# Kernel optimization log

Hardware: AMD Instinct MI355X
Metric: run time of the kernel (lower is better)

Reference implementation:

```python
import jax, jax.numpy as jnp
import numpy as np

NUM_USER = 100000
NUM_ITEM = 50000
EMBED_DIM = 64
NUM_LAYER = 3
NUM_INTERACTIONS = 1600000  # symmetrized -> nnz = 3.2M
BATCH = 4096


def setup_inputs() -> dict:
    key = jax.random.key(0)
    k1, k2, k3, k4, k5, k6 = jax.random.split(key, 6)
    N = NUM_USER + NUM_ITEM
    user_emb = jax.random.normal(k1, (NUM_USER, EMBED_DIM), dtype=jnp.float32) / EMBED_DIM
    item_emb = jax.random.normal(k2, (NUM_ITEM, EMBED_DIM), dtype=jnp.float32) / EMBED_DIM
    # random bipartite interactions, symmetrized adjacency
    u = jax.random.randint(k3, (NUM_INTERACTIONS,), 0, NUM_USER, dtype=jnp.int32)
    i = jax.random.randint(k4, (NUM_INTERACTIONS,), 0, NUM_ITEM, dtype=jnp.int32) + NUM_USER
    adj_rows = jnp.concatenate([u, i])  # [nnz]
    adj_cols = jnp.concatenate([i, u])  # [nnz]
    # symmetric normalization D^-1/2 A D^-1/2
    deg = jax.ops.segment_sum(jnp.ones_like(adj_rows, dtype=jnp.float32), adj_rows, num_segments=N)
    deg = jnp.maximum(deg, 1.0)
    inv_sqrt = 1.0 / jnp.sqrt(deg)
    adj_vals = inv_sqrt[adj_rows] * inv_sqrt[adj_cols]
    user_ids = jax.random.randint(k5, (BATCH,), 0, NUM_USER, dtype=jnp.int32)
    item_ids = jax.random.randint(k6, (BATCH,), 0, NUM_ITEM, dtype=jnp.int32)
    return {"user_emb": user_emb, "item_emb": item_emb, "adj_vals": adj_vals,
            "adj_rows": adj_rows, "adj_cols": adj_cols,
            "user_ids": user_ids, "item_ids": item_ids}


def reference(user_emb, item_emb, adj_vals, adj_rows, adj_cols, user_ids, item_ids):
    num_user = user_emb.shape[0]
    N = num_user + item_emb.shape[0]
    x = jnp.concatenate([user_emb, item_emb], axis=0)  # [N, D]
    acc = x  # running sum == stack+mean over layers, fused
    for _ in range(NUM_LAYER):
        # SpMM: out[r] += vals * x[c]
        x = jax.ops.segment_sum(adj_vals[:, None] * x[adj_cols], adj_rows, num_segments=N)
        acc = acc + x
    emb = acc / (NUM_LAYER + 1)
    batch_user = emb[user_ids]                  # [B, D]
    batch_item = emb[num_user + item_ids]       # [B, D]
    scores = jnp.sum(batch_user * batch_item, axis=-1)  # DotProdScorer
    return scores
```

## Files before the change

kernel.cpp:

```cpp
#include <hip/hip_runtime.h>


#define DIM 64
#define TSHIFT 8
#define TMASK ((1 << TSHIFT) - 1)
#define TPAD 768
#define EWG 6272
#define STAGE_CAP 6272
#define TSTRIDE 10240

typedef unsigned short u16;
typedef unsigned char u8;
typedef unsigned int u32;

__device__ __forceinline__ u32 f2bf(float f) {
  u32 u = __float_as_uint(f);
  return (u + 0x7FFFu + ((u >> 16) & 1u)) >> 16;
}
__device__ __forceinline__ float bflo(u32 u) {
  return __uint_as_float(u << 16);
}
__device__ __forceinline__ float bfhi(u32 u) {
  return __uint_as_float(u & 0xFFFF0000u);
}


__global__ __launch_bounds__(256) void partition_direct(
    const int* __restrict__ rows, const int* __restrict__ cols, int nnz,
    int T, int* __restrict__ tcur, u32* __restrict__ bucket) {
  __shared__ u32 sorted[STAGE_CAP];
  __shared__ u16 sortedt[STAGE_CAP];
  __shared__ int cnt[TPAD], lstart[TPAD], cur[TPAD], gbase[TPAD];
  __shared__ int hsum[256];
  int w = blockIdx.x, tid = threadIdx.x;
  int j0 = tid * 3;
  cnt[j0] = 0; cnt[j0 + 1] = 0; cnt[j0 + 2] = 0;
  cur[j0] = 0; cur[j0 + 1] = 0; cur[j0 + 2] = 0;
  __syncthreads();
  int base = w * EWG;
  int end = min(base + EWG, nnz);
  int total = end - base;
  if (total <= 0) return;
  for (int e = base + tid; e < end; e += 256)
    atomicAdd(&cnt[rows[e] >> TSHIFT], 1);
  __syncthreads();
  int c0 = cnt[j0], c1 = cnt[j0 + 1], c2 = cnt[j0 + 2];
  int lsum = c0 + c1 + c2;
  hsum[tid] = lsum;
  __syncthreads();
  for (int off = 1; off < 256; off <<= 1) {
    int v = (tid >= off) ? hsum[tid - off] : 0;
    __syncthreads();
    hsum[tid] += v;
    __syncthreads();
  }
  int excl = hsum[tid] - lsum;
  lstart[j0] = excl;
  lstart[j0 + 1] = excl + c0;
  lstart[j0 + 2] = excl + c0 + c1;
  if (c0 > 0) gbase[j0] = j0 * TSTRIDE + atomicAdd(&tcur[j0], c0);
  if (c1 > 0) gbase[j0 + 1] = (j0 + 1) * TSTRIDE + atomicAdd(&tcur[j0 + 1], c1);
  if (c2 > 0) gbase[j0 + 2] = (j0 + 2) * TSTRIDE + atomicAdd(&tcur[j0 + 2], c2);
  __syncthreads();
  for (int e = base + tid; e < end; e += 256) {
    int r = rows[e];
    int c = cols[e];
    int t = r >> TSHIFT;
    int slot = atomicAdd(&cur[t], 1);
    int d = lstart[t] + slot;
    sorted[d] = ((u32)(r & TMASK) << 18) | (u32)c;
    sortedt[d] = (u16)t;
  }
  __syncthreads();
  for (int i = tid; i < total; i += 256) {
    int t = sortedt[i];
    bucket[(size_t)gbase[t] + (i - lstart[t])] = sorted[i];
  }
}


__global__ __launch_bounds__(256) void build_csr_y0(
    const u32* __restrict__ bucket, const int* __restrict__ tcur, int T,
    int U, int N, const float4* __restrict__ ue, const float4* __restrict__ ie,
    int* __restrict__ row_ptr, u32* __restrict__ csr,
    uint4* __restrict__ y0b) {
  __shared__ int tl[TPAD];
  __shared__ int hist[256];
  __shared__ int sc[256];
  __shared__ int cur[256];
  int b = blockIdx.x;
  int t = (b & 1) ? (T - 1 - (b >> 1)) : (b >> 1);
  int tid = threadIdx.x;
  int j0 = tid * 3;
  int v0 = (j0 < T) ? tcur[j0] : 0;
  int v1 = (j0 + 1 < T) ? tcur[j0 + 1] : 0;
  int v2 = (j0 + 2 < T) ? tcur[j0 + 2] : 0;
  int lsum = v0 + v1 + v2;
  sc[tid] = lsum;
  __syncthreads();
  for (int off = 1; off < 256; off <<= 1) {
    int v = (tid >= off) ? sc[tid - off] : 0;
    __syncthreads();
    sc[tid] += v;
    __syncthreads();
  }
  int excl = sc[tid] - lsum;
  tl[j0] = excl + v0;
  tl[j0 + 1] = excl + v0 + v1;
  tl[j0 + 2] = excl + v0 + v1 + v2;
  hist[tid] = 0;
  __syncthreads();
  int tbase = (t == 0) ? 0 : tl[t - 1];
  int tlen = tl[t] - tbase;
  int bstart = t * TSTRIDE;
  const uint4* b4 = (const uint4*)(bucket + bstart);
  int nv = tlen >> 2;
  for (int i = tid; i < nv; i += 256) {
    uint4 e = b4[i];
    atomicAdd(&hist[e.x >> 18], 1);
    atomicAdd(&hist[e.y >> 18], 1);
    atomicAdd(&hist[e.z >> 18], 1);
    atomicAdd(&hist[e.w >> 18], 1);
  }
  for (int i = bstart + (nv << 2) + tid; i < bstart + tlen; i += 256)
    atomicAdd(&hist[bucket[i] >> 18], 1);
  __syncthreads();
  int h = hist[tid];
  sc[tid] = h;
  __syncthreads();
  for (int off = 1; off < 256; off <<= 1) {
    int v = (tid >= off) ? sc[tid - off] : 0;
    __syncthreads();
    sc[tid] += v;
    __syncthreads();
  }
  int incl = sc[tid];
  int r = (t << TSHIFT) + tid;
  if (r < N) row_ptr[r + 1] = tbase + incl;
  if (t == 0 && tid == 0) row_ptr[0] = 0;
  cur[tid] = tbase + incl - h;
  __syncthreads();
  for (int pass = 0; pass < 8; ++pass) {
    int lr = pass * 32 + (tid >> 3);
    int q = tid & 7;
    int row = (t << TSHIFT) + lr;
    if (row < N) {
      float invs = rsqrtf((float)max(hist[lr], 1));
      const float4* src = (row < U) ? (ue + (size_t)row * 16 + q * 2)
                                    : (ie + (size_t)(row - U) * 16 + q * 2);
      float4 a = src[0], bb = src[1];
      uint4 o;
      o.x = f2bf(a.x * invs) | (f2bf(a.y * invs) << 16);
      o.y = f2bf(a.z * invs) | (f2bf(a.w * invs) << 16);
      o.z = f2bf(bb.x * invs) | (f2bf(bb.y * invs) << 16);
      o.w = f2bf(bb.z * invs) | (f2bf(bb.w * invs) << 16);
      y0b[(size_t)row * 8 + q] = o;
    }
  }
  for (int i = tid; i < nv; i += 256) {
    uint4 e = b4[i];
    csr[atomicAdd(&cur[e.x >> 18], 1)] = e.x & 0x3FFFFu;
    csr[atomicAdd(&cur[e.y >> 18], 1)] = e.y & 0x3FFFFu;
    csr[atomicAdd(&cur[e.z >> 18], 1)] = e.z & 0x3FFFFu;
    csr[atomicAdd(&cur[e.w >> 18], 1)] = e.w & 0x3FFFFu;
  }
  for (int i = bstart + (nv << 2) + tid; i < bstart + tlen; i += 256) {
    u32 e = bucket[i];
    csr[atomicAdd(&cur[e >> 18], 1)] = e & 0x3FFFFu;
  }
}


#define ACC8(G)                                                              \
  s0 += bflo(G.x); s1 += bfhi(G.x);                                          \
  s2 += bflo(G.y); s3 += bfhi(G.y);                                          \
  s4 += bflo(G.z); s5 += bfhi(G.z);                                          \
  s6 += bflo(G.w); s7 += bfhi(G.w);

__global__ __launch_bounds__(256) void spmm_sum(
    const int* __restrict__ row_ptr, const u32* __restrict__ csr,
    const u16* __restrict__ yin, u16* __restrict__ yout, int n) {
  if (blockIdx.x == 0 && threadIdx.x < 8)
    ((uint4*)(yout + (size_t)n * DIM))[threadIdx.x] = make_uint4(0, 0, 0, 0);
  int row = (blockIdx.x * 256 + threadIdx.x) >> 3;
  int q8 = threadIdx.x & 7;
  if (row >= n) return;
  int start = row_ptr[row];
  int end = row_ptr[row + 1];
  float s0 = 0.f, s1 = 0.f, s2 = 0.f, s3 = 0.f;
  float s4 = 0.f, s5 = 0.f, s6 = 0.f, s7 = 0.f;
  int k = start;
  for (; k + 8 <= end; k += 8) {
    u32 c0 = csr[k],     c1 = csr[k + 1], c2 = csr[k + 2], c3 = csr[k + 3];
    u32 c4 = csr[k + 4], c5 = csr[k + 5], c6 = csr[k + 6], c7 = csr[k + 7];
    uint4 g0 = ((const uint4*)(yin + (size_t)c0 * DIM))[q8];
    uint4 g1 = ((const uint4*)(yin + (size_t)c1 * DIM))[q8];
    uint4 g2 = ((const uint4*)(yin + (size_t)c2 * DIM))[q8];
    uint4 g3 = ((const uint4*)(yin + (size_t)c3 * DIM))[q8];
    uint4 g4 = ((const uint4*)(yin + (size_t)c4 * DIM))[q8];
    uint4 g5 = ((const uint4*)(yin + (size_t)c5 * DIM))[q8];
    uint4 g6 = ((const uint4*)(yin + (size_t)c6 * DIM))[q8];
    uint4 g7 = ((const uint4*)(yin + (size_t)c7 * DIM))[q8];
    ACC8(g0) ACC8(g1) ACC8(g2) ACC8(g3) ACC8(g4) ACC8(g5) ACC8(g6) ACC8(g7)
  }
  for (; k + 4 <= end; k += 4) {
    u32 c0 = csr[k], c1 = csr[k + 1], c2 = csr[k + 2], c3 = csr[k + 3];
    uint4 g0 = ((const uint4*)(yin + (size_t)c0 * DIM))[q8];
    uint4 g1 = ((const uint4*)(yin + (size_t)c1 * DIM))[q8];
    uint4 g2 = ((const uint4*)(yin + (size_t)c2 * DIM))[q8];
    uint4 g3 = ((const uint4*)(yin + (size_t)c3 * DIM))[q8];
    ACC8(g0) ACC8(g1) ACC8(g2) ACC8(g3)
  }
  for (; k < end; ++k) {
    u32 c0 = csr[k];
    uint4 g0 = ((const uint4*)(yin + (size_t)c0 * DIM))[q8];
    ACC8(g0)
  }
  float inv = 1.0f / (float)max(end - start, 1);
  uint4 o;
  o.x = f2bf(s0 * inv) | (f2bf(s1 * inv) << 16);
  o.y = f2bf(s2 * inv) | (f2bf(s3 * inv) << 16);
  o.z = f2bf(s4 * inv) | (f2bf(s5 * inv) << 16);
  o.w = f2bf(s6 * inv) | (f2bf(s7 * inv) << 16);
  ((uint4*)(yout + (size_t)row * DIM))[q8] = o;
}


__device__ __forceinline__ void gather8(
    const int* __restrict__ row_ptr, const u32* __restrict__ csr,
    const u16* __restrict__ y, int row, int s, int q8, int n, float* o) {
  int start = row_ptr[row];
  int end = row_ptr[row + 1];
  float s0 = 0.f, s1 = 0.f, s2 = 0.f, s3 = 0.f;
  float s4 = 0.f, s5 = 0.f, s6 = 0.f, s7 = 0.f;
  for (int k = start + s; k < end; k += 16) {
    int k2 = k + 8;
    bool ok2 = k2 < end;
    u32 c0 = csr[k];
    u32 c1 = ok2 ? csr[k2] : (u32)n;
    uint4 g0 = ((const uint4*)(y + (size_t)c0 * DIM))[q8];
    uint4 g1 = ((const uint4*)(y + (size_t)c1 * DIM))[q8];
    ACC8(g0) ACC8(g1)
  }
  for (int m = 8; m <= 32; m <<= 1) {
    s0 += __shfl_xor(s0, m, 64); s1 += __shfl_xor(s1, m, 64);
    s2 += __shfl_xor(s2, m, 64); s3 += __shfl_xor(s3, m, 64);
    s4 += __shfl_xor(s4, m, 64); s5 += __shfl_xor(s5, m, 64);
    s6 += __shfl_xor(s6, m, 64); s7 += __shfl_xor(s7, m, 64);
  }
  o[0] = s0; o[1] = s1; o[2] = s2; o[3] = s3;
  o[4] = s4; o[5] = s5; o[6] = s6; o[7] = s7;
}

__global__ __launch_bounds__(256) void spmm3_score(
    const int* __restrict__ row_ptr, const u32* __restrict__ csr,
    const float* __restrict__ ue, const float* __restrict__ ie,
    const u16* __restrict__ y1b, const u16* __restrict__ y2b,
    const int* __restrict__ user_ids, const int* __restrict__ item_ids,
    int U, int N, int batch, float* __restrict__ out) {
  int w = (blockIdx.x * 256 + threadIdx.x) >> 6;
  int lane = threadIdx.x & 63;
  if (w >= batch) return;
  int s = lane >> 3;
  int q8 = lane & 7;
  int u = user_ids[w];
  int iti = item_ids[w];
  int it = iti + U;
  float gu[8], gi[8];
  gather8(row_ptr, csr, y2b, u, s, q8, N, gu);
  gather8(row_ptr, csr, y2b, it, s, q8, N, gi);
  int du = row_ptr[u + 1] - row_ptr[u];
  int di = row_ptr[it + 1] - row_ptr[it];
  float su = sqrtf((float)max(du, 1)), ru = 1.0f / su;
  float si = sqrtf((float)max(di, 1)), ri = 1.0f / si;
  const float4* pu = (const float4*)(ue + (size_t)u * DIM) + q8 * 2;
  const float4* pi = (const float4*)(ie + (size_t)iti * DIM) + q8 * 2;
  float4 a0a = pu[0], a0b = pu[1];
  float4 b0a = pi[0], b0b = pi[1];
  uint4 y1u = ((const uint4*)(y1b + (size_t)u * DIM))[q8];
  uint4 y2u = ((const uint4*)(y2b + (size_t)u * DIM))[q8];
  uint4 y1i = ((const uint4*)(y1b + (size_t)it * DIM))[q8];
  uint4 y2i = ((const uint4*)(y2b + (size_t)it * DIM))[q8];
  float a[8], b[8];
  a[0] = a0a.x + su * (bflo(y1u.x) + bflo(y2u.x)) + ru * gu[0];
  a[1] = a0a.y + su * (bfhi(y1u.x) + bfhi(y2u.x)) + ru * gu[1];
  a[2] = a0a.z + su * (bflo(y1u.y) + bflo(y2u.y)) + ru * gu[2];
  a[3] = a0a.w + su * (bfhi(y1u.y) + bfhi(y2u.y)) + ru * gu[3];
  a[4] = a0b.x + su * (bflo(y1u.z) + bflo(y2u.z)) + ru * gu[4];
  a[5] = a0b.y + su * (bfhi(y1u.z) + bfhi(y2u.z)) + ru * gu[5];
  a[6] = a0b.z + su * (bflo(y1u.w) + bflo(y2u.w)) + ru * gu[6];
  a[7] = a0b.w + su * (bfhi(y1u.w) + bfhi(y2u.w)) + ru * gu[7];
  b[0] = b0a.x + si * (bflo(y1i.x) + bflo(y2i.x)) + ri * gi[0];
  b[1] = b0a.y + si * (bfhi(y1i.x) + bfhi(y2i.x)) + ri * gi[1];
  b[2] = b0a.z + si * (bflo(y1i.y) + bflo(y2i.y)) + ri * gi[2];
  b[3] = b0a.w + si * (bfhi(y1i.y) + bfhi(y2i.y)) + ri * gi[3];
  b[4] = b0b.x + si * (bflo(y1i.z) + bflo(y2i.z)) + ri * gi[4];
  b[5] = b0b.y + si * (bfhi(y1i.z) + bfhi(y2i.z)) + ri * gi[5];
  b[6] = b0b.z + si * (bflo(y1i.w) + bflo(y2i.w)) + ri * gi[6];
  b[7] = b0b.w + si * (bfhi(y1i.w) + bfhi(y2i.w)) + ri * gi[7];
  float p = 0.f;
  for (int j = 0; j < 8; ++j) p += a[j] * b[j];
  p += __shfl_xor(p, 1, 64);
  p += __shfl_xor(p, 2, 64);
  p += __shfl_xor(p, 4, 64);
  if (lane == 0) out[w] = p * (1.0f / 16.0f);
}

extern "C" void kernel_launch(void* const* d_in, const int* in_sizes, int n_in,
                              void* d_out, int out_size, void* d_ws, size_t ws_size,
                              hipStream_t stream) {
  const float* user_emb = (const float*)d_in[0];
  const float* item_emb = (const float*)d_in[1];
  const int* adj_rows = (const int*)d_in[3];
  const int* adj_cols = (const int*)d_in[4];
  const int* user_ids = (const int*)d_in[5];
  const int* item_ids = (const int*)d_in[6];
  float* scores = (float*)d_out;

  const int U = in_sizes[0] / DIM;
  const int I = in_sizes[1] / DIM;
  const int N = U + I;
  const int nnz = in_sizes[2];
  const int B = in_sizes[5];

  const int T = (N + TMASK) >> TSHIFT;
  const int npw = (nnz + EWG - 1) / EWG;

  char* p = (char*)d_ws;
  auto carve = [&](size_t bytes) {
    void* r = (void*)p;
    p += (bytes + 255) & ~(size_t)255;
    return r;
  };
  u16* y0b = (u16*)carve((size_t)(N + 1) * DIM * 2);
  u16* y1b = (u16*)carve((size_t)(N + 1) * DIM * 2);
  u16* y2b = (u16*)carve((size_t)(N + 1) * DIM * 2);
  int* row_ptr = (int*)carve((size_t)(N + 1) * 4);
  int* tcur = (int*)carve((size_t)T * 4);
  u32* bucket = (u32*)carve((size_t)(T + 1) * TSTRIDE * 4);
  u32* csr = (u32*)carve((size_t)nnz * 4);

  hipMemsetAsync(tcur, 0, (size_t)T * 4, stream);

  partition_direct<<<npw, 256, 0, stream>>>(adj_rows, adj_cols, nnz, T, tcur,
                                            bucket);

  build_csr_y0<<<T, 256, 0, stream>>>(bucket, tcur, T, U, N,
                                      (const float4*)user_emb,
                                      (const float4*)item_emb, row_ptr,
                                      csr, (uint4*)y0b);

  const int sblocks = (N * 8 + 255) / 256;
  spmm_sum<<<sblocks, 256, 0, stream>>>(row_ptr, csr, y0b, y1b, N);
  spmm_sum<<<sblocks, 256, 0, stream>>>(row_ptr, csr, y1b, y2b, N);

  spmm3_score<<<(B + 3) / 4, 256, 0, stream>>>(row_ptr, csr, user_emb,
                                               item_emb, y1b, y2b, user_ids,
                                               item_ids, U, N, B, scores);
}
```

Before: 281.7 us.

## Use wave-shuffle block scans, vectorized partition loads, and smaller partition tiles

Replaces the shared-memory Hillis-Steele block scans, which carry many barriers, with a wave-level shuffle scan plus a small cross-wave combine in both preprocessing kernels. The partition kernel now reads rows and cols as int4, reuses the count array as the slot cursor, and shrinks the per-block edge chunk from 6272 to 2560 so more blocks fit per CU (launch bounds of 5). Smaller chunks mean more blocks and more global atomics on the tile cursors, and the int4 loads assume the chunk bases stay 16-byte aligned.

```diff
diff --git a/kernel.cpp b/kernel.cpp
--- a/kernel.cpp
+++ b/kernel.cpp
@@ -5,8 +5,8 @@
 #define TSHIFT 8
 #define TMASK ((1 << TSHIFT) - 1)
 #define TPAD 768
-#define EWG 6272
-#define STAGE_CAP 6272
+#define EWG 2560
+#define STAGE_CAP 2560
 #define TSTRIDE 10240
 
 typedef unsigned short u16;
@@ -24,50 +24,84 @@
   return __uint_as_float(u & 0xFFFF0000u);
 }
 
-
-__global__ __launch_bounds__(256) void partition_direct(
+__device__ __forceinline__ int block_incl_scan(int lsum, int tid, int* wsum) {
+  int lane = tid & 63, wv = tid >> 6;
+  int v = lsum;
+#pragma unroll
+  for (int off = 1; off < 64; off <<= 1) {
+    int t = __shfl_up(v, off, 64);
+    if (lane >= off) v += t;
+  }
+  __syncthreads();
+  if (lane == 63) wsum[wv] = v;
+  __syncthreads();
+  int add = 0;
+  if (wv > 0) add += wsum[0];
+  if (wv > 1) add += wsum[1];
+  if (wv > 2) add += wsum[2];
+  return v + add;
+}
+
+
+__global__ __launch_bounds__(256, 5) void partition_direct(
     const int* __restrict__ rows, const int* __restrict__ cols, int nnz,
     int T, int* __restrict__ tcur, u32* __restrict__ bucket) {
   __shared__ u32 sorted[STAGE_CAP];
   __shared__ u16 sortedt[STAGE_CAP];
-  __shared__ int cnt[TPAD], lstart[TPAD], cur[TPAD], gbase[TPAD];
-  __shared__ int hsum[256];
+  __shared__ int cnt[TPAD], lstart[TPAD], gbase[TPAD];
+  __shared__ int wsum[4];
   int w = blockIdx.x, tid = threadIdx.x;
   int j0 = tid * 3;
   cnt[j0] = 0; cnt[j0 + 1] = 0; cnt[j0 + 2] = 0;
-  cur[j0] = 0; cur[j0 + 1] = 0; cur[j0 + 2] = 0;
   __syncthreads();
   int base = w * EWG;
   int end = min(base + EWG, nnz);
   int total = end - base;
   if (total <= 0) return;
-  for (int e = base + tid; e < end; e += 256)
+  int nv = total >> 2;
+  const int4* r4 = (const int4*)(rows + base);
+  const int4* c4 = (const int4*)(cols + base);
+  for (int i = tid; i < nv; i += 256) {
+    int4 r = r4[i];
+    atomicAdd(&cnt[r.x >> TSHIFT], 1);
+    atomicAdd(&cnt[r.y >> TSHIFT], 1);
+    atomicAdd(&cnt[r.z >> TSHIFT], 1);
+    atomicAdd(&cnt[r.w >> TSHIFT], 1);
+  }
+  for (int e = base + (nv << 2) + tid; e < end; e += 256)
     atomicAdd(&cnt[rows[e] >> TSHIFT], 1);
   __syncthreads();
   int c0 = cnt[j0], c1 = cnt[j0 + 1], c2 = cnt[j0 + 2];
   int lsum = c0 + c1 + c2;
-  hsum[tid] = lsum;
-  __syncthreads();
-  for (int off = 1; off < 256; off <<= 1) {
-    int v = (tid >= off) ? hsum[tid - off] : 0;
-    __syncthreads();
-    hsum[tid] += v;
-    __syncthreads();
-  }
-  int excl = hsum[tid] - lsum;
+  int incl = block_incl_scan(lsum, tid, wsum);
+  int excl = incl - lsum;
   lstart[j0] = excl;
   lstart[j0 + 1] = excl + c0;
   lstart[j0 + 2] = excl + c0 + c1;
   if (c0 > 0) gbase[j0] = j0 * TSTRIDE + atomicAdd(&tcur[j0], c0);
   if (c1 > 0) gbase[j0 + 1] = (j0 + 1) * TSTRIDE + atomicAdd(&tcur[j0 + 1], c1);
   if (c2 > 0) gbase[j0 + 2] = (j0 + 2) * TSTRIDE + atomicAdd(&tcur[j0 + 2], c2);
-  __syncthreads();
-  for (int e = base + tid; e < end; e += 256) {
+  cnt[j0] = 0; cnt[j0 + 1] = 0; cnt[j0 + 2] = 0;
+  __syncthreads();
+  for (int i = tid; i < nv; i += 256) {
+    int4 r = r4[i];
+    int4 c = c4[i];
+    int t, s, d;
+    t = r.x >> TSHIFT; s = atomicAdd(&cnt[t], 1); d = lstart[t] + s;
+    sorted[d] = ((u32)(r.x & TMASK) << 18) | (u32)c.x; sortedt[d] = (u16)t;
+    t = r.y >> TSHIFT; s = atomicAdd(&cnt[t], 1); d = lstart[t] + s;
+    sorted[d] = ((u32)(r.y & TMASK) << 18) | (u32)c.y; sortedt[d] = (u16)t;
+    t = r.z >> TSHIFT; s = atomicAdd(&cnt[t], 1); d = lstart[t] + s;
+    sorted[d] = ((u32)(r.z & TMASK) << 18) | (u32)c.z; sortedt[d] = (u16)t;
+    t = r.w >> TSHIFT; s = atomicAdd(&cnt[t], 1); d = lstart[t] + s;
+    sorted[d] = ((u32)(r.w & TMASK) << 18) | (u32)c.w; sortedt[d] = (u16)t;
+  }
+  for (int e = base + (nv << 2) + tid; e < end; e += 256) {
     int r = rows[e];
     int c = cols[e];
     int t = r >> TSHIFT;
-    int slot = atomicAdd(&cur[t], 1);
-    int d = lstart[t] + slot;
+    int s = atomicAdd(&cnt[t], 1);
+    int d = lstart[t] + s;
     sorted[d] = ((u32)(r & TMASK) << 18) | (u32)c;
     sortedt[d] = (u16)t;
   }
@@ -86,8 +120,8 @@
     uint4* __restrict__ y0b) {
   __shared__ int tl[TPAD];
   __shared__ int hist[256];
-  __shared__ int sc[256];
   __shared__ int cur[256];
+  __shared__ int wsum[4];
   int b = blockIdx.x;
   int t = (b & 1) ? (T - 1 - (b >> 1)) : (b >> 1);
   int tid = threadIdx.x;
@@ -96,18 +130,11 @@
   int v1 = (j0 + 1 < T) ? tcur[j0 + 1] : 0;
   int v2 = (j0 + 2 < T) ? tcur[j0 + 2] : 0;
   int lsum = v0 + v1 + v2;
-  sc[tid] = lsum;
-  __syncthreads();
-  for (int off = 1; off < 256; off <<= 1) {
-    int v = (tid >= off) ? sc[tid - off] : 0;
-    __syncthreads();
-    sc[tid] += v;
-    __syncthreads();
-  }
-  int excl = sc[tid] - lsum;
-  tl[j0] = excl + v0;
-  tl[j0 + 1] = excl + v0 + v1;
-  tl[j0 + 2] = excl + v0 + v1 + v2;
+  int incl0 = block_incl_scan(lsum, tid, wsum);
+  int excl0 = incl0 - lsum;
+  tl[j0] = excl0 + v0;
+  tl[j0 + 1] = excl0 + v0 + v1;
+  tl[j0 + 2] = excl0 + v0 + v1 + v2;
   hist[tid] = 0;
   __syncthreads();
   int tbase = (t == 0) ? 0 : tl[t - 1];
@@ -126,15 +153,7 @@
     atomicAdd(&hist[bucket[i] >> 18], 1);
   __syncthreads();
   int h = hist[tid];
-  sc[tid] = h;
-  __syncthreads();
-  for (int off = 1; off < 256; off <<= 1) {
-    int v = (tid >= off) ? sc[tid - off] : 0;
-    __syncthreads();
-    sc[tid] += v;
-    __syncthreads();
-  }
-  int incl = sc[tid];
+  int incl = block_incl_scan(h, tid, wsum);
   int r = (t << TSHIFT) + tid;
   if (r < N) row_ptr[r + 1] = tbase + incl;
   if (t == 0 && tid == 0) row_ptr[0] = 0;
```

New measurement: 302.0 us. 1.07x slower.
